# Kernel tuning notes

Measured on AMD Instinct MI355X. Metric: run time of the kernel, lower is better.

## Reference

```python
import jax, jax.numpy as jnp
import numpy as np

N_QUBITS = 4


def _apply_rx(state, theta, wire):
    # state: [B, 2,2,2,2] complex64, theta: [B] real angles; RX on `wire`.
    st = jnp.moveaxis(state, wire + 1, -1)
    bshape = (theta.shape[0],) + (1,) * (st.ndim - 2)
    c = jnp.cos(theta * 0.5).reshape(bshape).astype(jnp.complex64)
    s = (-1j) * jnp.sin(theta * 0.5).reshape(bshape).astype(jnp.complex64)
    new = jnp.stack([c * st[..., 0] + s * st[..., 1],
                     s * st[..., 0] + c * st[..., 1]], axis=-1)
    return jnp.moveaxis(new, -1, wire + 1)


def _apply_cnot(state, control, target):
    st = jnp.moveaxis(state, (control + 1, target + 1), (-2, -1))
    new = jnp.stack([st[..., 0, :], st[..., 1, ::-1]], axis=-2)
    return jnp.moveaxis(new, (-2, -1), (control + 1, target + 1))


def _quantum_gate(angles, thetas):
    # angles: [B, n] data-encoding RX angles; thetas: [n] trainable RX angles.
    B, n = angles.shape
    state = jnp.zeros((B,) + (2,) * n, jnp.complex64)
    state = state.at[(slice(None),) + (0,) * n].set(1.0)  # |0...0>
    for w in range(n):
        state = _apply_rx(state, angles[:, w], w)
    for w in range(n):
        state = _apply_rx(state, jnp.broadcast_to(thetas[w], (B,)), w)
    for w in range(n):
        state = _apply_cnot(state, w, (w + 1) % n)
    probs = jnp.abs(state.reshape(B, 2 ** n)) ** 2  # [B, 16]
    bits = (np.arange(2 ** n)[:, None] >> np.arange(n - 1, -1, -1)[None, :]) & 1
    signs = jnp.asarray(1.0 - 2.0 * bits, jnp.float32)  # [16, n] PauliZ eigvals
    return probs @ signs  # [B, n] <Z_w> expectations


def setup_inputs() -> dict:
    key = jax.random.key(0)
    ks = jax.random.split(key, 12)
    B, D, H, n = 131072, 256, 4, N_QUBITS
    fan_in = D + H
    sc = 1.0 / np.sqrt(fan_in)
    inp = {
        'x': jax.random.normal(ks[0], (B, D), jnp.float32),
        'hx': jax.random.normal(ks[1], (B, H), jnp.float32),
        'cx': jax.random.normal(ks[2], (B, H), jnp.float32),
        'W_f': jax.random.normal(ks[3], (n, fan_in), jnp.float32) * sc,
        'b_f': jnp.zeros((n,), jnp.float32),
        'W_i': jax.random.normal(ks[4], (n, fan_in), jnp.float32) * sc,
        'b_i': jnp.zeros((n,), jnp.float32),
        'W_u': jax.random.normal(ks[5], (n, fan_in), jnp.float32) * sc,
        'b_u': jnp.zeros((n,), jnp.float32),
        'W_o': jax.random.normal(ks[6], (n, fan_in), jnp.float32) * sc,
        'b_o': jnp.zeros((n,), jnp.float32),
        'th_f': jax.random.normal(ks[7], (n,), jnp.float32),
        'th_i': jax.random.normal(ks[8], (n,), jnp.float32),
        'th_u': jax.random.normal(ks[9], (n,), jnp.float32),
        'th_o': jax.random.normal(ks[10], (n,), jnp.float32),
    }
    return inp


def reference(x, hx, cx, W_f, b_f, W_i, b_i, W_u, b_u, W_o, b_o,
              th_f, th_i, th_u, th_o):
    comb = jnp.concatenate([x, hx], axis=1)  # [B, D+H]
    f = jax.nn.sigmoid(_quantum_gate(comb @ W_f.T + b_f, th_f))
    i = jax.nn.sigmoid(_quantum_gate(comb @ W_i.T + b_i, th_i))
    g = jnp.tanh(_quantum_gate(comb @ W_u.T + b_u, th_u))
    o = jax.nn.sigmoid(_quantum_gate(comb @ W_o.T + b_o, th_o))
    c_new = f * cx + i * g
    h_new = o * jnp.tanh(c_new)
    return (h_new, c_new)
```

## Files before the change

### kernel.cpp

```cpp
#include <hip/hip_runtime.h>

#define NB    131072
#define TPB   64
#define FANIN 260

__device__ __forceinline__ float sigm_(float x) { return 1.0f / (1.0f + __expf(-x)); }
__device__ __forceinline__ float tanh_(float x) { return 1.0f - 2.0f / (__expf(2.0f * x) + 1.0f); }

__device__ __forceinline__ void gld_lds16(const float4* gsrc, float4* ldst) {
    __builtin_amdgcn_global_load_lds(
        (const __attribute__((address_space(1))) void*)gsrc,
        (__attribute__((address_space(3))) void*)ldst, 16, 0, 0);
}

__global__ void qlstm_prep(const float* __restrict__ Wf, const float* __restrict__ bf,
                           const float* __restrict__ Wi, const float* __restrict__ bi,
                           const float* __restrict__ Wu, const float* __restrict__ bu,
                           const float* __restrict__ Wo, const float* __restrict__ bo,
                           const float* __restrict__ thf, const float* __restrict__ thi,
                           const float* __restrict__ thu, const float* __restrict__ tho,
                           float* __restrict__ Wp, float* __restrict__ bth) {
    int t = blockIdx.x * blockDim.x + threadIdx.x;
    if (t < FANIN * 16) {
        int k = t >> 4, gw = t & 15, g = gw >> 2, w = gw & 3;
        const float* Wg = (g == 0) ? Wf : (g == 1) ? Wi : (g == 2) ? Wu : Wo;
        Wp[t] = Wg[w * FANIN + k];
    }
    if (t < 16) {
        int g = t >> 2, w = t & 3;
        const float* bg = (g == 0) ? bf  : (g == 1) ? bi  : (g == 2) ? bu  : bo;
        const float* tg = (g == 0) ? thf : (g == 1) ? thi : (g == 2) ? thu : tho;
        bth[t] = bg[w] + tg[w];
    }
}

__global__ __launch_bounds__(TPB, 2) void qlstm_main(
        const float* __restrict__ x, const float* __restrict__ hx,
        const float* __restrict__ cx, const float* __restrict__ Wp,
        const float* __restrict__ bth, float* __restrict__ out) {
    __shared__ float4 xs4[2 * TPB * 8];

    const int lane = threadIdx.x;
    const int row0 = blockIdx.x * TPB;
    const int row  = row0 + lane;
    const float4* x4 = (const float4*)x;

    float4 hv  = ((const float4*)hx)[row];
    float4 cxv = ((const float4*)cx)[row];

    const int rsub = lane >> 3;
    const int csw  = (lane & 7) ^ rsub;
    const size_t gbase = (size_t)(row0 + rsub) * 64 + csw;

#pragma unroll
    for (int u = 0; u < 8; ++u)
        gld_lds16(x4 + gbase + (size_t)u * 8 * 64, &xs4[u * 64]);

    float acc[16];
#pragma unroll
    for (int j = 0; j < 16; ++j) acc[j] = 0.0f;

#pragma unroll 2
    for (int stage = 0; stage < 8; ++stage) {
        const int cb = (stage & 1) * (TPB * 8);

        if (stage < 7) {
            const int nb_ = ((stage + 1) & 1) * (TPB * 8);
#pragma unroll
            for (int u = 0; u < 8; ++u)
                gld_lds16(x4 + gbase + (size_t)(stage + 1) * 8 + (size_t)u * 8 * 64,
                          &xs4[nb_ + u * 64]);
            asm volatile("s_waitcnt vmcnt(8)" ::: "memory");
        } else {
            asm volatile("s_waitcnt vmcnt(0)" ::: "memory");
        }

        const float* wbase = Wp + stage * 32 * 16;
#pragma unroll
        for (int k4 = 0; k4 < 8; ++k4) {
            float4 xv = xs4[cb + lane * 8 + (k4 ^ (lane & 7))];
#pragma unroll
            for (int m = 0; m < 4; ++m) {
                float xe = (m == 0) ? xv.x : (m == 1) ? xv.y
                         : (m == 2) ? xv.z : xv.w;
                const float* wp = wbase + (k4 * 4 + m) * 16;
#pragma unroll
                for (int j = 0; j < 16; ++j) acc[j] = fmaf(xe, wp[j], acc[j]);
            }
        }
    }

    {
        const float* wp = Wp + 256 * 16;
#pragma unroll
        for (int j = 0; j < 16; ++j) acc[j] = fmaf(hv.x, wp[j],      acc[j]);
#pragma unroll
        for (int j = 0; j < 16; ++j) acc[j] = fmaf(hv.y, wp[16 + j], acc[j]);
#pragma unroll
        for (int j = 0; j < 16; ++j) acc[j] = fmaf(hv.z, wp[32 + j], acc[j]);
#pragma unroll
        for (int j = 0; j < 16; ++j) acc[j] = fmaf(hv.w, wp[48 + j], acc[j]);
    }

    float co[16];
#pragma unroll
    for (int j = 0; j < 16; ++j) co[j] = __cosf(acc[j] + bth[j]);

    float G[16];
#pragma unroll
    for (int g = 0; g < 4; ++g) {
        float c0 = co[g * 4 + 0], c1 = co[g * 4 + 1];
        float c2 = co[g * 4 + 2], c3 = co[g * 4 + 3];
        float e1 = c0 * c1;
        float e2 = e1 * c2;
        float e3 = e2 * c3;
        float e0 = c1 * c2 * c3;
        G[g * 4 + 0] = e0; G[g * 4 + 1] = e1; G[g * 4 + 2] = e2; G[g * 4 + 3] = e3;
    }

    float cxa[4] = {cxv.x, cxv.y, cxv.z, cxv.w};
    float hn[4], cn[4];
#pragma unroll
    for (int w = 0; w < 4; ++w) {
        float fg = sigm_(G[0 * 4 + w]);
        float ig = sigm_(G[1 * 4 + w]);
        float ug = tanh_(G[2 * 4 + w]);
        float og = sigm_(G[3 * 4 + w]);
        float c_ = fg * cxa[w] + ig * ug;
        cn[w] = c_;
        hn[w] = og * tanh_(c_);
    }

    ((float4*)out)[row]      = make_float4(hn[0], hn[1], hn[2], hn[3]);
    ((float4*)out)[NB + row] = make_float4(cn[0], cn[1], cn[2], cn[3]);
}

extern "C" void kernel_launch(void* const* d_in, const int* in_sizes, int n_in,
                              void* d_out, int out_size, void* d_ws, size_t ws_size,
                              hipStream_t stream) {
    const float* x   = (const float*)d_in[0];
    const float* hx  = (const float*)d_in[1];
    const float* cx  = (const float*)d_in[2];
    const float* Wf  = (const float*)d_in[3];
    const float* bf  = (const float*)d_in[4];
    const float* Wi  = (const float*)d_in[5];
    const float* bi  = (const float*)d_in[6];
    const float* Wu  = (const float*)d_in[7];
    const float* bu  = (const float*)d_in[8];
    const float* Wo  = (const float*)d_in[9];
    const float* bo  = (const float*)d_in[10];
    const float* thf = (const float*)d_in[11];
    const float* thi = (const float*)d_in[12];
    const float* thu = (const float*)d_in[13];
    const float* tho = (const float*)d_in[14];

    float* Wp  = (float*)d_ws;
    float* bth = Wp + FANIN * 16;

    qlstm_prep<<<(FANIN * 16 + 255) / 256, 256, 0, stream>>>(
        Wf, bf, Wi, bi, Wu, bu, Wo, bo, thf, thi, thu, tho, Wp, bth);

    qlstm_main<<<NB / TPB, TPB, 0, stream>>>(
        x, hx, cx, Wp, bth, (float*)d_out);
}
```

Baseline: 241.2 us.

## Split GEMV across waves with K-partitioned reduction and separate tail kernel

Replaces the one-row-per-thread kernel with a persistent 512-thread GEMV kernel. Each of the 8 waves handles a slice of the 256-wide K dimension for 64-row tiles, and partial sums are reduced through LDS, with x streamed through double-buffered direct global-to-LDS loads. Pre-activations are written to workspace, and a second kernel adds the hx contribution and applies the quantum-gate cosine products and LSTM nonlinearities. This aims to raise occupancy and memory-level parallelism for streaming x, at the cost of an extra workspace round trip, an extra launch and many block barriers.

```diff
diff --git a/kernel.cpp b/kernel.cpp
--- a/kernel.cpp
+++ b/kernel.cpp
@@ -1,16 +1,18 @@
 #include <hip/hip_runtime.h>
 
 #define NB    131072
-#define TPB   64
+#define TPB   512
+#define NBLK  512
+#define TILES 4
 #define FANIN 260
 
 __device__ __forceinline__ float sigm_(float x) { return 1.0f / (1.0f + __expf(-x)); }
 __device__ __forceinline__ float tanh_(float x) { return 1.0f - 2.0f / (__expf(2.0f * x) + 1.0f); }
 
-__device__ __forceinline__ void gld_lds16(const float4* gsrc, float4* ldst) {
+__device__ __forceinline__ void gld_lds16(const float4* g, float4* l) {
     __builtin_amdgcn_global_load_lds(
-        (const __attribute__((address_space(1))) void*)gsrc,
-        (__attribute__((address_space(3))) void*)ldst, 16, 0, 0);
+        (const __attribute__((address_space(1))) void*)g,
+        (__attribute__((address_space(3))) void*)l, 16, 0, 0);
 }
 
 __global__ void qlstm_prep(const float* __restrict__ Wf, const float* __restrict__ bf,
@@ -34,62 +36,128 @@
     }
 }
 
-__global__ __launch_bounds__(TPB, 2) void qlstm_main(
-        const float* __restrict__ x, const float* __restrict__ hx,
+__global__ __launch_bounds__(TPB, 4) void qlstm_gemv(
+        const float* __restrict__ x, const float* __restrict__ Wp,
+        float4* __restrict__ wsAcc ) {
+    __shared__ float4 xb0[64 * 16];
+    __shared__ float4 xb1[64 * 16];
+    __shared__ float4 ex4[4 * 4 * 64];
+
+    const int tid  = threadIdx.x;
+    const int lane = tid & 63;
+    const int wvu  = __builtin_amdgcn_readfirstlane(tid >> 6);
+    const int brow0 = blockIdx.x * (TILES * 64);
+
+    const float4* x4 = (const float4*)x;
+
+    const int r0 = 4 * (wvu * 2 + 0) + (lane >> 4);
+    const int r1 = 4 * (wvu * 2 + 1) + (lane >> 4);
+    const int c0 = (lane & 15) ^ (r0 & 7);
+    const int c1 = (lane & 15) ^ (r1 & 7);
+
+#define ISSUE_UNIT(TT, QQ, DST) do {                                                   \
+        gld_lds16(x4 + (size_t)(brow0 + (TT) * 64 + r0) * 64 + (QQ) * 16 + c0,         \
+                  &(DST)[(wvu * 2 + 0) * 64]);                                         \
+        gld_lds16(x4 + (size_t)(brow0 + (TT) * 64 + r1) * 64 + (QQ) * 16 + c1,         \
+                  &(DST)[(wvu * 2 + 1) * 64]);                                         \
+    } while (0)
+
+    ISSUE_UNIT(0, 0, xb0);
+    ISSUE_UNIT(0, 1, xb1);
+
+    float acc[16];
+#pragma unroll
+    for (int j = 0; j < 16; ++j) acc[j] = 0.0f;
+
+    for (int tau = 0; tau < TILES; ++tau) {
+#pragma unroll
+        for (int q = 0; q < 4; ++q) {
+            if (q < 2 && wvu == 0 && tau > 0)
+                asm volatile("s_waitcnt vmcnt(6)" ::: "memory");
+            else
+                asm volatile("s_waitcnt vmcnt(2)" ::: "memory");
+            __builtin_amdgcn_s_barrier();
+
+            const float4* pb = (q & 1) ? xb1 : xb0;
+#pragma unroll
+            for (int j = 0; j < 2; ++j) {
+                float4 xv = pb[lane * 16 + ((wvu * 2 + j) ^ (lane & 7))];
+                const float* wp = Wp + (q * 16 + wvu * 2 + j) * 64;
+#pragma unroll
+                for (int m = 0; m < 4; ++m) {
+                    float xe = (m == 0) ? xv.x : (m == 1) ? xv.y
+                             : (m == 2) ? xv.z : xv.w;
+#pragma unroll
+                    for (int jj = 0; jj < 16; ++jj)
+                        acc[jj] = fmaf(xe, wp[m * 16 + jj], acc[jj]);
+                }
+            }
+            __builtin_amdgcn_s_barrier();
+            if (tau < TILES - 1 || q < 2) {
+                const int u2 = tau * 4 + q + 2;
+                if (q & 1) ISSUE_UNIT(u2 >> 2, u2 & 3, xb1);
+                else       ISSUE_UNIT(u2 >> 2, u2 & 3, xb0);
+            }
+        }
+
+        if (wvu >= 4) {
+#pragma unroll
+            for (int j4 = 0; j4 < 4; ++j4)
+                ex4[(j4 * 4 + (wvu - 4)) * 64 + lane] =
+                    make_float4(acc[j4 * 4 + 0], acc[j4 * 4 + 1],
+                                acc[j4 * 4 + 2], acc[j4 * 4 + 3]);
+        }
+        __builtin_amdgcn_s_barrier();
+        if (wvu < 4) {
+#pragma unroll
+            for (int j4 = 0; j4 < 4; ++j4) {
+                float4 p = ex4[(j4 * 4 + wvu) * 64 + lane];
+                acc[j4 * 4 + 0] += p.x; acc[j4 * 4 + 1] += p.y;
+                acc[j4 * 4 + 2] += p.z; acc[j4 * 4 + 3] += p.w;
+            }
+        }
+        if (wvu >= 1 && wvu < 4) {
+#pragma unroll
+            for (int j4 = 0; j4 < 4; ++j4)
+                ex4[(j4 * 4 + wvu) * 64 + lane] =
+                    make_float4(acc[j4 * 4 + 0], acc[j4 * 4 + 1],
+                                acc[j4 * 4 + 2], acc[j4 * 4 + 3]);
+        }
+        __builtin_amdgcn_s_barrier();
+        if (wvu == 0) {
+#pragma unroll
+            for (int j4 = 0; j4 < 4; ++j4) {
+                float4 p1 = ex4[(j4 * 4 + 1) * 64 + lane];
+                float4 p2 = ex4[(j4 * 4 + 2) * 64 + lane];
+                float4 p3 = ex4[(j4 * 4 + 3) * 64 + lane];
+                wsAcc[(size_t)j4 * NB + brow0 + tau * 64 + lane] =
+                    make_float4(acc[j4 * 4 + 0] + p1.x + p2.x + p3.x,
+                                acc[j4 * 4 + 1] + p1.y + p2.y + p3.y,
+                                acc[j4 * 4 + 2] + p1.z + p2.z + p3.z,
+                                acc[j4 * 4 + 3] + p1.w + p2.w + p3.w);
+            }
+        }
+#pragma unroll
+        for (int j = 0; j < 16; ++j) acc[j] = 0.0f;
+    }
+#undef ISSUE_UNIT
+}
+
+__global__ __launch_bounds__(256) void qlstm_tail(
+        const float4* __restrict__ wsAcc, const float* __restrict__ hx,
         const float* __restrict__ cx, const float* __restrict__ Wp,
         const float* __restrict__ bth, float* __restrict__ out) {
-    __shared__ float4 xs4[2 * TPB * 8];
-
-    const int lane = threadIdx.x;
-    const int row0 = blockIdx.x * TPB;
-    const int row  = row0 + lane;
-    const float4* x4 = (const float4*)x;
-
-    float4 hv  = ((const float4*)hx)[row];
-    float4 cxv = ((const float4*)cx)[row];
-
-    const int rsub = lane >> 3;
-    const int csw  = (lane & 7) ^ rsub;
-    const size_t gbase = (size_t)(row0 + rsub) * 64 + csw;
-
-#pragma unroll
-    for (int u = 0; u < 8; ++u)
-        gld_lds16(x4 + gbase + (size_t)u * 8 * 64, &xs4[u * 64]);
+    const int row = blockIdx.x * 256 + threadIdx.x;
 
     float acc[16];
 #pragma unroll
-    for (int j = 0; j < 16; ++j) acc[j] = 0.0f;
-
-#pragma unroll 2
-    for (int stage = 0; stage < 8; ++stage) {
-        const int cb = (stage & 1) * (TPB * 8);
-
-        if (stage < 7) {
-            const int nb_ = ((stage + 1) & 1) * (TPB * 8);
-#pragma unroll
-            for (int u = 0; u < 8; ++u)
-                gld_lds16(x4 + gbase + (size_t)(stage + 1) * 8 + (size_t)u * 8 * 64,
-                          &xs4[nb_ + u * 64]);
-            asm volatile("s_waitcnt vmcnt(8)" ::: "memory");
-        } else {
-            asm volatile("s_waitcnt vmcnt(0)" ::: "memory");
-        }
-
-        const float* wbase = Wp + stage * 32 * 16;
-#pragma unroll
-        for (int k4 = 0; k4 < 8; ++k4) {
-            float4 xv = xs4[cb + lane * 8 + (k4 ^ (lane & 7))];
-#pragma unroll
-            for (int m = 0; m < 4; ++m) {
-                float xe = (m == 0) ? xv.x : (m == 1) ? xv.y
-                         : (m == 2) ? xv.z : xv.w;
-                const float* wp = wbase + (k4 * 4 + m) * 16;
-#pragma unroll
-                for (int j = 0; j < 16; ++j) acc[j] = fmaf(xe, wp[j], acc[j]);
-            }
-        }
-    }
-
+    for (int j4 = 0; j4 < 4; ++j4) {
+        float4 a = wsAcc[(size_t)j4 * NB + row];
+        acc[j4 * 4 + 0] = a.x; acc[j4 * 4 + 1] = a.y;
+        acc[j4 * 4 + 2] = a.z; acc[j4 * 4 + 3] = a.w;
+    }
+
+    float4 hv = ((const float4*)hx)[row];
     {
         const float* wp = Wp + 256 * 16;
 #pragma unroll
@@ -118,6 +186,7 @@
         G[g * 4 + 0] = e0; G[g * 4 + 1] = e1; G[g * 4 + 2] = e2; G[g * 4 + 3] = e3;
     }
 
+    float4 cxv = ((const float4*)cx)[row];
     float cxa[4] = {cxv.x, cxv.y, cxv.z, cxv.w};
     float hn[4], cn[4];
 #pragma unroll
@@ -154,12 +223,14 @@
     const float* thu = (const float*)d_in[13];
     const float* tho = (const float*)d_in[14];
 
-    float* Wp  = (float*)d_ws;
-    float* bth = Wp + FANIN * 16;
+    float*  Wp    = (float*)d_ws;
+    float*  bth   = Wp + FANIN * 16;
+    float4* wsAcc = (float4*)((char*)d_ws + 32768);
 
     qlstm_prep<<<(FANIN * 16 + 255) / 256, 256, 0, stream>>>(
         Wf, bf, Wi, bi, Wu, bu, Wo, bo, thf, thi, thu, tho, Wp, bth);
 
-    qlstm_main<<<NB / TPB, TPB, 0, stream>>>(
-        x, hx, cx, Wp, bth, (float*)d_out);
-}
+    qlstm_gemv<<<NBLK, TPB, 0, stream>>>(x, Wp, wsAcc);
+
+    qlstm_tail<<<NB / 256, 256, 0, stream>>>(wsAcc, hx, cx, Wp, bth, (float*)d_out);
+}
```

After: 234.8 us. 2.6% less time.
